# Optimization experiments

Hardware: AMD Instinct MI355X
Metric: run time of the kernel (lower is better)

## Reference

```python
import jax, jax.numpy as jnp
import numpy as np

B, F, T, K = 16, 256, 2048, 20
TEMP = 0.5
EPS = 1e-8  # torch cosine_similarity eps


def setup_inputs() -> dict:
    key = jax.random.key(0)
    k1, k2, k3 = jax.random.split(key, 3)
    z = jax.random.normal(k1, (B, F, T), dtype=jnp.float32)
    c = jax.random.normal(k2, (B, F, T + 1), dtype=jnp.float32)
    # torch: torch.randint(0, full_len - 1, size=(B, T * K))  -> values in [0, T-2]
    negative_inds = jax.random.randint(k3, (B, T * K), 0, T - 1, dtype=jnp.int64)
    return {"z": z, "c": c, "negative_inds": negative_inds}


def reference(z, c, negative_inds):
    # ---- _generate_negatives ----
    # z: [B, F, T] -> flat rows [B*T, F]
    z_flat = jnp.transpose(z, (0, 2, 1)).reshape(-1, F)
    # per-batch offset i*T (torch adds it in-place for i in 1..B-1)
    inds = negative_inds + (jnp.arange(B, dtype=negative_inds.dtype) * T)[:, None]
    negatives = z_flat[inds.reshape(-1)].reshape(B, T, K, F)

    # ---- _calculate_similarity ----
    c_t = jnp.transpose(c[..., 1:], (0, 2, 1))[:, :, None, :]  # [B, T, 1, F] (drop start token)
    z_t = jnp.transpose(z, (0, 2, 1))[:, :, None, :]           # [B, T, 1, F]
    neg_is_pos = jnp.all(c_t == negatives, axis=-1)            # [B, T, K]
    targets = jnp.concatenate([c_t, negatives], axis=-2)       # [B, T, K+1, F]

    num = jnp.sum(z_t * targets, axis=-1)                      # [B, T, K+1]
    denom = jnp.maximum(
        jnp.linalg.norm(z_t, axis=-1) * jnp.linalg.norm(targets, axis=-1), EPS
    )
    logits = (num / denom) / TEMP                              # [B, T, K+1]

    # mask negatives that exactly equal the positive (wav2vec2-style)
    pad = jnp.zeros_like(neg_is_pos[..., :1])
    full_mask = jnp.concatenate([pad, neg_is_pos], axis=-1)    # [B, T, K+1]
    logits = jnp.where(full_mask, -jnp.inf, logits)

    return logits.reshape(-1, K + 1)                           # [B*T, K+1]
```

## Files before the change

### kernel.cpp

```cpp
#include <hip/hip_runtime.h>
#include <hip/hip_fp16.h>
#include <math.h>

#define B_ 16
#define F_ 256
#define T_ 2048
#define K_ 20
#define OUTK 21
#define NPAIR 10

typedef _Float16 half2v __attribute__((ext_vector_type(2)));
typedef float v2f __attribute__((ext_vector_type(2)));

#if __has_builtin(__builtin_amdgcn_cvt_pk_f32_fp8) && __has_builtin(__builtin_amdgcn_cvt_pk_fp8_f32)
#define HW_FP8 1
#else
#define HW_FP8 0
#endif

#if !HW_FP8
__device__ __forceinline__ float dec_fp8(unsigned v) {
    unsigned s = (v >> 7) & 1, e = (v >> 3) & 15, m = v & 7;
    float r = e ? __uint_as_float(((e + 120u) << 23) | (m << 20))
                : (float)m * 0.001953125f;
    return s ? -r : r;
}
__device__ __forceinline__ unsigned enc_fp8(float x) {
    unsigned bits = __float_as_uint(x);
    unsigned s = bits >> 31;
    unsigned a = bits & 0x7fffffffu;
    float ax = __uint_as_float(a);
    unsigned r;
    if (ax < 0.015625f) {
        r = (unsigned)(int)(ax * 512.f + 0.5f);
    } else {
        int e = (int)(a >> 23) - 127;
        unsigned m = a & 0x7fffffu;
        unsigned keep = m >> 20, rest = m & 0xFFFFFu;
        keep += (rest > 0x80000u) || (rest == 0x80000u && (keep & 1));
        if (keep == 8) { keep = 0; ++e; }
        r = ((unsigned)(e + 7) << 3) | keep;
    }
    return (s << 7) | r;
}
#endif

__device__ __forceinline__ unsigned pack_fp8x2(float a0, float a1) {
#if HW_FP8
    return (unsigned)__builtin_amdgcn_cvt_pk_fp8_f32(a0, a1, 0, false) & 0xFFFFu;
#else
    return enc_fp8(a0) | (enc_fp8(a1) << 8);
#endif
}
template <bool HI>
__device__ __forceinline__ v2f unpk_fp8(unsigned u) {
#if HW_FP8
    return __builtin_amdgcn_cvt_pk_f32_fp8((int)u, HI);
#else
    v2f r; unsigned x = HI ? (u >> 16) : u;
    r[0] = dec_fp8(x & 0xFF); r[1] = dec_fp8((x >> 8) & 0xFF);
    return r;
#endif
}

__global__ __launch_bounds__(256) void prep_kernel(
    const float* __restrict__ z, const float* __restrict__ c,
    ushort* __restrict__ zth, unsigned char* __restrict__ zf8,
    unsigned char* __restrict__ cf8)
{
    __shared__ float tile[256][33];
    __shared__ float sc[32];
    int which = blockIdx.z;
    const float* src = which ? c : z;
    int Lsrc = which ? (T_ + 1) : T_;
    int co   = which;

    int b  = blockIdx.y;
    int t0 = blockIdx.x * 32;
    const float* srcb = src + (size_t)b * F_ * Lsrc;
    int tl = threadIdx.x & 31;
    int fl = threadIdx.x >> 5;
#pragma unroll
    for (int i = 0; i < 32; ++i) {
        int f = i * 8 + fl;
        tile[f][tl] = srcb[(size_t)f * Lsrc + (t0 + tl + co)];
    }
    __syncthreads();
    if (threadIdx.x < 32) {
        float s = 0.f;
#pragma unroll 8
        for (int f = 0; f < 256; ++f) { float v = tile[f][threadIdx.x]; s += v * v; }
        float n = sqrtf(s);
        sc[threadIdx.x] = (n > 0.f) ? (1.0f / n) : 0.f;
    }
    __syncthreads();
    int l   = threadIdx.x & 127;
    int rhi = threadIdx.x >> 7;
    if (which == 0) {
#pragma unroll
        for (int j2 = 0; j2 < 16; ++j2) {
            int row = j2 * 2 + rhi;
            float s  = sc[row];
            float a  = tile[2 * l][row] * s;
            float bb = tile[2 * l + 1][row] * s;
            unsigned u = ((unsigned)__half_as_ushort(__float2half(bb)) << 16)
                       |  (unsigned)__half_as_ushort(__float2half(a));
            ((unsigned*)(zth + ((size_t)b * T_ + t0 + row) * F_))[l] = u;
            ((ushort*)(zf8 + ((size_t)b * T_ + t0 + row) * F_))[l] =
                (ushort)pack_fp8x2(a, bb);
        }
    } else {
#pragma unroll
        for (int j2 = 0; j2 < 16; ++j2) {
            int row = j2 * 2 + rhi;
            float s  = sc[row];
            float a  = tile[2 * l][row] * s;
            float bb = tile[2 * l + 1][row] * s;
            ((ushort*)(cf8 + ((size_t)b * T_ + t0 + row) * F_))[l] =
                (ushort)pack_fp8x2(a, bb);
        }
    }
}

__device__ __forceinline__ float dpp_half_sum(float x) {
    x += __int_as_float(__builtin_amdgcn_mov_dpp(__float_as_int(x), 0x111, 0xF, 0xF, true));
    x += __int_as_float(__builtin_amdgcn_mov_dpp(__float_as_int(x), 0x112, 0xF, 0xF, true));
    x += __int_as_float(__builtin_amdgcn_mov_dpp(__float_as_int(x), 0x114, 0xF, 0xF, true));
    x += __int_as_float(__builtin_amdgcn_mov_dpp(__float_as_int(x), 0x118, 0xF, 0xF, true));
    x += __int_as_float(__builtin_amdgcn_mov_dpp(__float_as_int(x), 0x142, 0xF, 0xF, true));
    return x;
}

__global__ __launch_bounds__(256, 8) void sim_kernel(
    const ushort* __restrict__ zth, const unsigned char* __restrict__ zf8,
    const unsigned char* __restrict__ cf8, const int* __restrict__ inds,
    float* __restrict__ out)
{
    __shared__ float sd[128];
    int i = blockIdx.x;
    int b = (i & 7) | ((i >= 4096) ? 8 : 0);
    int wid = threadIdx.x >> 6;
    int t = (((i >> 3) & 511) << 2) + wid;
    int lane = threadIdx.x & 63;
    int hl = lane & 31;
    int hi = lane >> 5;
    int bt = __builtin_amdgcn_readfirstlane((b << 11) + t);

    const int* myinds = inds + bt * K_;
    int idxv = myinds[(lane < K_) ? lane : 0];

    uint4 zv  = ((const uint4*)(zth + (size_t)bt * F_))[hl];
    uint2 cv8 = ((const uint2*)(cf8 + (size_t)bt * F_))[hl];

    const char* tbl8 = (const char*)zf8;
    unsigned zbase8  = (unsigned)(b << 11) * 256u;
    unsigned laneoff = (unsigned)hl * 8u;

    uint2 tv[NPAIR];
#pragma unroll
    for (int p = 0; p < NPAIR; ++p) {
        unsigned ilo = (unsigned)__builtin_amdgcn_readlane(idxv, 2 * p);
        unsigned ihi = (unsigned)__builtin_amdgcn_readlane(idxv, 2 * p + 1);
        unsigned off = zbase8 + (hi ? ihi : ilo) * 256u + laneoff;
        tv[p] = *(const uint2*)(tbl8 + off);
    }

    __builtin_amdgcn_sched_barrier(0);

    float zf[8];
    {
        unsigned uu[4] = {zv.x, zv.y, zv.z, zv.w};
#pragma unroll
        for (int q = 0; q < 4; ++q) {
            half2v h = __builtin_bit_cast(half2v, uu[q]);
            zf[2 * q] = (float)h[0]; zf[2 * q + 1] = (float)h[1];
        }
    }

    float dc;
    {
        v2f c01 = unpk_fp8<false>(cv8.x);
        v2f c23 = unpk_fp8<true >(cv8.x);
        v2f c45 = unpk_fp8<false>(cv8.y);
        v2f c67 = unpk_fp8<true >(cv8.y);
        float d = zf[0] * c01[0];
        d = fmaf(zf[1], c01[1], d);
        d = fmaf(zf[2], c23[0], d);
        d = fmaf(zf[3], c23[1], d);
        d = fmaf(zf[4], c45[0], d);
        d = fmaf(zf[5], c45[1], d);
        d = fmaf(zf[6], c67[0], d);
        d = fmaf(zf[7], c67[1], d);
        dc = d;
    }

    float dz[NPAIR];
#pragma unroll
    for (int p = 0; p < NPAIR; ++p) {
        v2f t01 = unpk_fp8<false>(tv[p].x);
        v2f t23 = unpk_fp8<true >(tv[p].x);
        v2f t45 = unpk_fp8<false>(tv[p].y);
        v2f t67 = unpk_fp8<true >(tv[p].y);
        float d = zf[0] * t01[0];
        d = fmaf(zf[1], t01[1], d);
        d = fmaf(zf[2], t23[0], d);
        d = fmaf(zf[3], t23[1], d);
        d = fmaf(zf[4], t45[0], d);
        d = fmaf(zf[5], t45[1], d);
        d = fmaf(zf[6], t67[0], d);
        d = fmaf(zf[7], t67[1], d);
        dz[p] = d;
    }

    unsigned mb = 0;
#pragma unroll
    for (int p = 0; p < NPAIR; ++p) {
        unsigned long long ball = __ballot(tv[p].x == cv8.x);
        unsigned blo = (unsigned)ball, bhi = (unsigned)(ball >> 32);
        if (blo == 0xFFFFFFFFu || bhi == 0xFFFFFFFFu) {
            bool full = (tv[p].x == cv8.x) && (tv[p].y == cv8.y);
            unsigned long long b2 = __ballot(full);
            if ((unsigned)b2 == 0xFFFFFFFFu)          mb |= 1u << (1 + 2 * p);
            if ((unsigned)(b2 >> 32) == 0xFFFFFFFFu)  mb |= 1u << (2 + 2 * p);
        }
    }

    dc = dpp_half_sum(dc);
#pragma unroll
    for (int p = 0; p < NPAIR; ++p) dz[p] = dpp_half_sum(dz[p]);

    if (hl == 31) {
        if (hi == 0) sd[wid * 32] = dc;
#pragma unroll
        for (int p = 0; p < NPAIR; ++p) sd[wid * 32 + 1 + 2 * p + hi] = dz[p];
    }

    if (lane < OUTK) {
        float v = sd[wid * 32 + lane] * 2.0f;
        if ((mb >> lane) & 1u) v = -INFINITY;
        out[(size_t)bt * OUTK + lane] = v;
    }
}

extern "C" void kernel_launch(void* const* d_in, const int* in_sizes, int n_in,
                              void* d_out, int out_size, void* d_ws, size_t ws_size,
                              hipStream_t stream)
{
    const float* z    = (const float*)d_in[0];
    const float* c    = (const float*)d_in[1];
    const int*   inds = (const int*)d_in[2];
    float* out = (float*)d_out;

    char* ws = (char*)d_ws;
    size_t f16_bytes = (size_t)B_ * T_ * F_ * sizeof(ushort);
    size_t f8_bytes  = (size_t)B_ * T_ * F_;
    ushort* zth = (ushort*)ws;
    unsigned char* zf8 = (unsigned char*)(ws + f16_bytes);
    unsigned char* cf8 = (unsigned char*)(ws + f16_bytes + f8_bytes);

    dim3 tb(256), tg(T_ / 32, B_, 2);
    prep_kernel<<<tg, tb, 0, stream>>>(z, c, zth, zf8, cf8);
    sim_kernel<<<dim3(B_ * T_ / 4), dim3(256), 0, stream>>>(zth, zf8, cf8, inds, out);
}
```

Before: 46.76 us.

## Drop fp16 z copy, use fp8 for anchor, parallelize norm reduction, pack fp8x4

The separate fp16 copy of normalized z is removed, so the anchor vector is now also read from the fp8 table. This saves 16 MB of workspace writes in prep and halves the anchor read in sim. The prep norm computation is split across all 256 threads with a two-stage reduction through shared memory, and stores use 4-byte fp8x4 words. The trade-off is lower anchor precision (fp8 instead of fp16), which raises the dot-product error. The new fp8x4 store layout is consistent with how sim unpacks the data.

Result: faster. 42.52 us (-9.1%).

```diff
diff --git a/kernel.cpp b/kernel.cpp
--- a/kernel.cpp
+++ b/kernel.cpp
@@ -9,7 +9,6 @@
 #define OUTK 21
 #define NPAIR 10
 
-typedef _Float16 half2v __attribute__((ext_vector_type(2)));
 typedef float v2f __attribute__((ext_vector_type(2)));
 
 #if __has_builtin(__builtin_amdgcn_cvt_pk_f32_fp8) && __has_builtin(__builtin_amdgcn_cvt_pk_fp8_f32)
@@ -45,11 +44,14 @@
 }
 #endif
 
-__device__ __forceinline__ unsigned pack_fp8x2(float a0, float a1) {
+__device__ __forceinline__ unsigned pack_fp8x4(float a0, float a1, float a2, float a3) {
 #if HW_FP8
-    return (unsigned)__builtin_amdgcn_cvt_pk_fp8_f32(a0, a1, 0, false) & 0xFFFFu;
+    int u = 0;
+    u = __builtin_amdgcn_cvt_pk_fp8_f32(a0, a1, u, false);
+    u = __builtin_amdgcn_cvt_pk_fp8_f32(a2, a3, u, true);
+    return (unsigned)u;
 #else
-    return enc_fp8(a0) | (enc_fp8(a1) << 8);
+    return enc_fp8(a0) | (enc_fp8(a1) << 8) | (enc_fp8(a2) << 16) | (enc_fp8(a3) << 24);
 #endif
 }
 template <bool HI>
@@ -65,13 +67,14 @@
 
 __global__ __launch_bounds__(256) void prep_kernel(
     const float* __restrict__ z, const float* __restrict__ c,
-    ushort* __restrict__ zth, unsigned char* __restrict__ zf8,
-    unsigned char* __restrict__ cf8)
+    unsigned char* __restrict__ zf8, unsigned char* __restrict__ cf8)
 {
     __shared__ float tile[256][33];
+    __shared__ float ps[32][9];
     __shared__ float sc[32];
     int which = blockIdx.z;
     const float* src = which ? c : z;
+    unsigned char* dst = which ? cf8 : zf8;
     int Lsrc = which ? (T_ + 1) : T_;
     int co   = which;
 
@@ -86,38 +89,34 @@
         tile[f][tl] = srcb[(size_t)f * Lsrc + (t0 + tl + co)];
     }
     __syncthreads();
+    {
+        int col = threadIdx.x & 31, oct = threadIdx.x >> 5;
+        float s = 0.f;
+#pragma unroll 8
+        for (int q = 0; q < 32; ++q) {
+            float v = tile[oct * 32 + q][col];
+            s = fmaf(v, v, s);
+        }
+        ps[col][oct] = s;
+    }
+    __syncthreads();
     if (threadIdx.x < 32) {
         float s = 0.f;
-#pragma unroll 8
-        for (int f = 0; f < 256; ++f) { float v = tile[f][threadIdx.x]; s += v * v; }
+#pragma unroll
+        for (int o = 0; o < 8; ++o) s += ps[threadIdx.x][o];
         float n = sqrtf(s);
         sc[threadIdx.x] = (n > 0.f) ? (1.0f / n) : 0.f;
     }
     __syncthreads();
-    int l   = threadIdx.x & 127;
-    int rhi = threadIdx.x >> 7;
-    if (which == 0) {
-#pragma unroll
-        for (int j2 = 0; j2 < 16; ++j2) {
-            int row = j2 * 2 + rhi;
-            float s  = sc[row];
-            float a  = tile[2 * l][row] * s;
-            float bb = tile[2 * l + 1][row] * s;
-            unsigned u = ((unsigned)__half_as_ushort(__float2half(bb)) << 16)
-                       |  (unsigned)__half_as_ushort(__float2half(a));
-            ((unsigned*)(zth + ((size_t)b * T_ + t0 + row) * F_))[l] = u;
-            ((ushort*)(zf8 + ((size_t)b * T_ + t0 + row) * F_))[l] =
-                (ushort)pack_fp8x2(a, bb);
-        }
-    } else {
-#pragma unroll
-        for (int j2 = 0; j2 < 16; ++j2) {
-            int row = j2 * 2 + rhi;
-            float s  = sc[row];
-            float a  = tile[2 * l][row] * s;
-            float bb = tile[2 * l + 1][row] * s;
-            ((ushort*)(cf8 + ((size_t)b * T_ + t0 + row) * F_))[l] =
-                (ushort)pack_fp8x2(a, bb);
+    {
+        int j = threadIdx.x & 63, r4 = threadIdx.x >> 6;
+#pragma unroll
+        for (int it = 0; it < 8; ++it) {
+            int row = it * 4 + r4;
+            float s = sc[row];
+            unsigned u = pack_fp8x4(tile[2 * j][row] * s, tile[2 * j + 1][row] * s,
+                                    tile[2 * j + 128][row] * s, tile[2 * j + 129][row] * s);
+            ((unsigned*)(dst + ((size_t)b * T_ + t0 + row) * F_))[j] = u;
         }
     }
 }
@@ -132,9 +131,8 @@
 }
 
 __global__ __launch_bounds__(256, 8) void sim_kernel(
-    const ushort* __restrict__ zth, const unsigned char* __restrict__ zf8,
-    const unsigned char* __restrict__ cf8, const int* __restrict__ inds,
-    float* __restrict__ out)
+    const unsigned char* __restrict__ zf8, const unsigned char* __restrict__ cf8,
+    const int* __restrict__ inds, float* __restrict__ out)
 {
     __shared__ float sd[128];
     int i = blockIdx.x;
@@ -149,7 +147,7 @@
     const int* myinds = inds + bt * K_;
     int idxv = myinds[(lane < K_) ? lane : 0];
 
-    uint4 zv  = ((const uint4*)(zth + (size_t)bt * F_))[hl];
+    uint2 zv8 = ((const uint2*)(zf8 + (size_t)bt * F_))[hl];
     uint2 cv8 = ((const uint2*)(cf8 + (size_t)bt * F_))[hl];
 
     const char* tbl8 = (const char*)zf8;
@@ -169,20 +167,16 @@
 
     float zf[8];
     {
-        unsigned uu[4] = {zv.x, zv.y, zv.z, zv.w};
-#pragma unroll
-        for (int q = 0; q < 4; ++q) {
-            half2v h = __builtin_bit_cast(half2v, uu[q]);
-            zf[2 * q] = (float)h[0]; zf[2 * q + 1] = (float)h[1];
-        }
+        v2f a01 = unpk_fp8<false>(zv8.x), a23 = unpk_fp8<true>(zv8.x);
+        v2f a45 = unpk_fp8<false>(zv8.y), a67 = unpk_fp8<true>(zv8.y);
+        zf[0] = a01[0]; zf[1] = a01[1]; zf[2] = a23[0]; zf[3] = a23[1];
+        zf[4] = a45[0]; zf[5] = a45[1]; zf[6] = a67[0]; zf[7] = a67[1];
     }
 
     float dc;
     {
-        v2f c01 = unpk_fp8<false>(cv8.x);
-        v2f c23 = unpk_fp8<true >(cv8.x);
-        v2f c45 = unpk_fp8<false>(cv8.y);
-        v2f c67 = unpk_fp8<true >(cv8.y);
+        v2f c01 = unpk_fp8<false>(cv8.x), c23 = unpk_fp8<true>(cv8.x);
+        v2f c45 = unpk_fp8<false>(cv8.y), c67 = unpk_fp8<true>(cv8.y);
         float d = zf[0] * c01[0];
         d = fmaf(zf[1], c01[1], d);
         d = fmaf(zf[2], c23[0], d);
@@ -197,10 +191,8 @@
     float dz[NPAIR];
 #pragma unroll
     for (int p = 0; p < NPAIR; ++p) {
-        v2f t01 = unpk_fp8<false>(tv[p].x);
-        v2f t23 = unpk_fp8<true >(tv[p].x);
-        v2f t45 = unpk_fp8<false>(tv[p].y);
-        v2f t67 = unpk_fp8<true >(tv[p].y);
+        v2f t01 = unpk_fp8<false>(tv[p].x), t23 = unpk_fp8<true>(tv[p].x);
+        v2f t45 = unpk_fp8<false>(tv[p].y), t67 = unpk_fp8<true>(tv[p].y);
         float d = zf[0] * t01[0];
         d = fmaf(zf[1], t01[1], d);
         d = fmaf(zf[2], t23[0], d);
@@ -252,13 +244,11 @@
     float* out = (float*)d_out;
 
     char* ws = (char*)d_ws;
-    size_t f16_bytes = (size_t)B_ * T_ * F_ * sizeof(ushort);
-    size_t f8_bytes  = (size_t)B_ * T_ * F_;
-    ushort* zth = (ushort*)ws;
-    unsigned char* zf8 = (unsigned char*)(ws + f16_bytes);
-    unsigned char* cf8 = (unsigned char*)(ws + f16_bytes + f8_bytes);
+    size_t f8_bytes = (size_t)B_ * T_ * F_;
+    unsigned char* zf8 = (unsigned char*)ws;
+    unsigned char* cf8 = (unsigned char*)(ws + f8_bytes);
 
     dim3 tb(256), tg(T_ / 32, B_, 2);
-    prep_kernel<<<tg, tb, 0, stream>>>(z, c, zth, zf8, cf8);
-    sim_kernel<<<dim3(B_ * T_ / 4), dim3(256), 0, stream>>>(zth, zf8, cf8, inds, out);
-}
+    prep_kernel<<<tg, tb, 0, stream>>>(z, c, zf8, cf8);
+    sim_kernel<<<dim3(B_ * T_ / 4), dim3(256), 0, stream>>>(zf8, cf8, inds, out);
+}
```
